# Kernel optimization log

Hardware: AMD Instinct MI355X
Metric: run time of the kernel (lower is better)

Reference implementation:

```python
import jax, jax.numpy as jnp
import numpy as np

EPS = float(jnp.finfo(jnp.float32).eps)


def _mlp(x, W1, b1, W2, b2, W3, b3):
    h = jax.nn.relu(x @ W1 + b1)
    h = jax.nn.relu(h @ W2 + b2)
    return h @ W3 + b3


def setup_inputs() -> dict:
    B, D_A, D_B, K, H = 131072, 16, 16, 32, 256
    key = jax.random.key(0)
    ks = jax.random.split(key, 13)
    def lin(k, fi, fo):
        return jax.random.normal(k, (fi, fo), jnp.float32) * (fi ** -0.5)
    inp = {
        "x": jax.random.uniform(ks[0], (B, D_A + D_B), jnp.float32),
        "hW1": lin(ks[1], D_A, H), "hb1": jnp.zeros((H,), jnp.float32),
        "hW2": lin(ks[2], H, H),   "hb2": jnp.zeros((H,), jnp.float32),
        "hW3": lin(ks[3], H, D_B * (K + 1)), "hb3": jnp.zeros((D_B * (K + 1),), jnp.float32),
        "wW1": lin(ks[4], D_A, H), "wb1": jnp.zeros((H,), jnp.float32),
        "wW2": lin(ks[5], H, H),   "wb2": jnp.zeros((H,), jnp.float32),
        "wW3": lin(ks[6], H, D_B * K), "wb3": jnp.zeros((D_B * K,), jnp.float32),
        "A_dims": jnp.arange(0, 32, 2, dtype=jnp.int32),
        "B_dims": jnp.arange(1, 32, 2, dtype=jnp.int32),
    }
    return inp


def reference(x, hW1, hb1, hW2, hb2, hW3, hb3, wW1, wb1, wW2, wb2, wW3, wb3, A_dims, B_dims):
    B = x.shape[0]
    D_B = B_dims.shape[0]
    K = wW3.shape[1] // D_B
    x_A = x[:, A_dims]               # (B, D_A)
    x_B = x[:, B_dims]               # (B, D_B)

    raw_h = _mlp(x_A, hW1, hb1, hW2, hb2, hW3, hb3).reshape(B, D_B, K + 1)
    heights = jax.nn.softplus(raw_h) + EPS
    raw_w = _mlp(x_A, wW1, wb1, wW2, wb2, wW3, wb3).reshape(B, D_B, K)
    widths = jax.nn.softmax(raw_w, axis=-1)
    zeros = jnp.zeros((B, D_B, 1), x.dtype)
    bins = jnp.concatenate([zeros, jnp.cumsum(widths, axis=-1)], axis=-1)  # (B, D_B, K+1)

    # preprocess_params_2: normalise PDF heights and bin areas
    bin_widths = bins[:, :, 1:] - bins[:, :, :-1]
    bin_areas = 0.5 * (heights[:, :, :-1] + heights[:, :, 1:]) * bin_widths  # (B, D_B, K)
    total_area = bin_areas.sum(axis=-1, keepdims=True)
    v = heights / total_area
    bin_areas = bin_areas / total_area

    # bin search
    i = jnp.sum(x_B[..., None] >= bins, axis=-1) - 1
    i = jnp.clip(i, 0, K - 1)                                  # (B, D_B)
    iu = i[..., None]

    x_left = jnp.take_along_axis(bins, iu, axis=2)[..., 0]
    x_right = jnp.take_along_axis(bins, iu + 1, axis=2)[..., 0]
    w_b = x_right - x_left
    v_left = jnp.take_along_axis(v, iu, axis=2)[..., 0]
    v_right = jnp.take_along_axis(v, iu + 1, axis=2)[..., 0]
    w_v = v_right - v_left

    alpha = (x_B - x_left) / (w_b + EPS)
    # cumulative area up to left edge of bin i: exclusive prefix sum then gather
    c_edges = jnp.concatenate([zeros, jnp.cumsum(bin_areas, axis=-1)], axis=-1)
    c_left = jnp.take_along_axis(c_edges, iu, axis=2)[..., 0]

    y_B = c_left + 0.5 * alpha ** 2 * w_v * w_b + alpha * v_left * w_b
    y = x.at[:, B_dims].set(y_B)
    return y
```

## Files before the change

kernel.cpp:

```cpp
#include <hip/hip_runtime.h>
#include <cmath>

typedef short short8 __attribute__((ext_vector_type(8)));
typedef short short4v __attribute__((ext_vector_type(4)));
typedef float f32x16 __attribute__((ext_vector_type(16)));

#define EPSF 1.1920929e-07f

#define LDS_A2W 0
#define LDS_A2H 33792
#define LDS_EW  67584
#define LDS_HH  104448
#define LDS_XA  67584
#define LDS_A1  69632
#define LDS_TOTAL 141312

#define OFF1H 0
#define OFF1W 4096
#define OFF2H 8192
#define OFF2W 73728
#define OFF3H 139264
#define OFF3W 278528

__device__ __forceinline__ unsigned short f2bf(float f) {
  union { float f; unsigned u; } v; v.f = f;
  return (unsigned short)((v.u + 0x8000u) >> 16);
}
__device__ __forceinline__ float bf2f(unsigned short h) {
  union { unsigned u; float f; } v; v.u = ((unsigned)h) << 16; return v.f;
}

__global__ void pack_weights(const float* __restrict__ hW1, const float* __restrict__ wW1,
                             const float* __restrict__ hW2, const float* __restrict__ wW2,
                             const float* __restrict__ hW3, const float* __restrict__ wW3,
                             unsigned short* __restrict__ out) {
  int tile = blockIdx.x, l = threadIdx.x;
  const float* src; unsigned short* dst; int NT, N, K, base;
  if (tile < 8)        { src = hW1; dst = out + OFF1H; NT = 8;  N = 256; K = 16;  base = tile; }
  else if (tile < 16)  { src = wW1; dst = out + OFF1W; NT = 8;  N = 256; K = 16;  base = tile - 8; }
  else if (tile < 144) { src = hW2; dst = out + OFF2H; NT = 8;  N = 256; K = 256; base = tile - 16; }
  else if (tile < 272) { src = wW2; dst = out + OFF2W; NT = 8;  N = 256; K = 256; base = tile - 144; }
  else if (tile < 544) { src = hW3; dst = out + OFF3H; NT = 17; N = 528; K = 256; base = tile - 272; }
  else                 { src = wW3; dst = out + OFF3W; NT = 16; N = 512; K = 256; base = tile - 544; }
  int nt = base % NT, kt = base / NT;
  int n = nt * 32 + (l & 31);
  int k0 = kt * 16 + (l >> 5) * 8;
  short8 v;
  #pragma unroll
  for (int e = 0; e < 8; e++) {
    float f = (n < N && (k0 + e) < K) ? src[(k0 + e) * N + n] : 0.f;
    v[e] = (short)f2bf(f);
  }
  *(short8*)(dst + (base * 64 + l) * 8) = v;
}

template <int KT, int NTB>
__device__ __forceinline__ f32x16 gemm_tile(const unsigned short* __restrict__ A, int apitch,
                                            const unsigned short* __restrict__ pB, int ct) {
  int l = threadIdx.x & 63;
  f32x16 acc = {0.f,0.f,0.f,0.f,0.f,0.f,0.f,0.f,0.f,0.f,0.f,0.f,0.f,0.f,0.f,0.f};
  const unsigned short* aptr = A + (l & 31) * apitch + (l >> 5) * 8;
  const unsigned short* bptr = pB + (ct * 64 + l) * 8;
  #pragma unroll
  for (int kt = 0; kt < KT; kt++) {
    short8 b = *(const short8*)(bptr + kt * (NTB * 512));
    short8 a = *(const short8*)(aptr + kt * 16);
    acc = __builtin_amdgcn_mfma_f32_32x32x16_bf16(a, b, acc, 0, 0, 0);
  }
  return acc;
}

__device__ __forceinline__ void epi_relu(char* lds, int oOff, f32x16 acc,
                                         const float* __restrict__ bias, int rt, int ct) {
  int l = threadIdx.x & 63;
  int col = ct * 32 + (l & 31);
  float bv = bias[col];
  unsigned short* o = (unsigned short*)(lds + oOff) + col + (rt * 32 + 4 * (l >> 5)) * 264;
  #pragma unroll
  for (int r = 0; r < 16; r++) {
    int row = (r & 3) + 8 * (r >> 2);
    o[row * 264] = f2bf(fmaxf(acc[r] + bv, 0.f));
  }
}

__global__ __launch_bounds__(1024, 4) void fused_kernel(
    const float* __restrict__ x,
    const float* __restrict__ hb1, const float* __restrict__ hb2, const float* __restrict__ hb3,
    const float* __restrict__ wb1, const float* __restrict__ wb2, const float* __restrict__ wb3,
    const unsigned short* __restrict__ pw,
    float* __restrict__ y) {
  extern __shared__ char lds[];
  const int t = threadIdx.x;
  const int w = t >> 6, l = t & 63;
  const int r0 = blockIdx.x * 64;

  if (t < 512) {
    int row = t >> 3, c4 = t & 7;
    float4 v = *(const float4*)(x + (r0 + row) * 32 + c4 * 4);
    y[(r0 + row) * 32 + c4 * 4] = v.x;
    y[(r0 + row) * 32 + c4 * 4 + 2] = v.z;
    unsigned short* xa = (unsigned short*)(lds + LDS_XA) + row * 16 + c4 * 2;
    xa[0] = f2bf(v.x); xa[1] = f2bf(v.z);
  }
  __syncthreads();

  const int rt = w >> 3, ct = w & 7;
  const unsigned short* XA = (const unsigned short*)(lds + LDS_XA);
  const unsigned short* A1 = (const unsigned short*)(lds + LDS_A1);
  const unsigned short* A2W = (const unsigned short*)(lds + LDS_A2W);
  const unsigned short* A2H = (const unsigned short*)(lds + LDS_A2H);

  { f32x16 a = gemm_tile<1, 8>(XA + rt * 32 * 16, 16, pw + OFF1W, ct);
    epi_relu(lds, LDS_A1, a, wb1, rt, ct); }
  __syncthreads();
  { f32x16 a = gemm_tile<16, 8>(A1 + rt * 32 * 264, 264, pw + OFF2W, ct);
    epi_relu(lds, LDS_A2W, a, wb2, rt, ct); }
  __syncthreads();
  { f32x16 a = gemm_tile<1, 8>(XA + rt * 32 * 16, 16, pw + OFF1H, ct);
    epi_relu(lds, LDS_A1, a, hb1, rt, ct); }
  __syncthreads();
  { f32x16 a = gemm_tile<16, 8>(A1 + rt * 32 * 264, 264, pw + OFF2H, ct);
    epi_relu(lds, LDS_A2H, a, hb2, rt, ct); }
  __syncthreads();

  #pragma unroll 1
  for (int H = 0; H < 2; H++) {
    for (int u = w; u < 34; u += 16) {
      int urt = u & 1, q = u >> 1;
      int rbase = urt * 32 + 4 * (l >> 5);
      if (q < 8) {
        int ctg = H * 8 + q;
        f32x16 a = gemm_tile<16, 16>(A2W + urt * 32 * 264, 264, pw + OFF3W, ctg);
        int c = ctg * 32 + (l & 31);
        float bv = wb3[c];
        unsigned short* o = (unsigned short*)(lds + LDS_EW) + rbase * 288 + (ctg & 7) * 36 + (l & 31);
        #pragma unroll
        for (int r = 0; r < 16; r++) {
          int row = (r & 3) + 8 * (r >> 2);
          o[row * 288] = f2bf(__expf(a[r] + bv));
        }
      } else {
        int ctg = (q - 8) + 8 * H;
        f32x16 a = gemm_tile<16, 17>(A2H + urt * 32 * 264, 264, pw + OFF3H, ctg);
        int c = ctg * 32 + (l & 31);
        if (c >= 264 * H && c < 264 * (H + 1)) {
          float bv = hb3[c];
          unsigned d = ((unsigned)c * 993u) >> 15;
          int j = c - 33 * (int)d;
          unsigned short* o = (unsigned short*)(lds + LDS_HH) + rbase * 288 + ((int)d & 7) * 36 + j;
          #pragma unroll
          for (int r = 0; r < 16; r++) {
            int row = (r & 3) + 8 * (r >> 2);
            float v = a[r] + bv;
            float sp = fmaxf(v, 0.f) + __logf(1.f + __expf(-fabsf(v))) + EPSF;
            o[row * 288] = f2bf(sp);
          }
        }
      }
    }
    __syncthreads();

    {
      int p = t >> 1, half = t & 1;
      int row = p >> 3, dl = p & 7, dg = H * 8 + dl;
      const unsigned short* EWp = (const unsigned short*)(lds + LDS_EW) + row * 288 + dl * 36 + half * 16;
      const unsigned short* HHp = (const unsigned short*)(lds + LDS_HH) + row * 288 + dl * 36 + half * 16;
      float e[16], hh[17];
      #pragma unroll
      for (int i = 0; i < 4; i++) {
        short4v ev = *(const short4v*)(EWp + i * 4);
        short4v hv = *(const short4v*)(HHp + i * 4);
        #pragma unroll
        for (int jj = 0; jj < 4; jj++) {
          e[i * 4 + jj] = bf2f((unsigned short)ev[jj]);
          hh[i * 4 + jj] = bf2f((unsigned short)hv[jj]);
        }
      }
      hh[16] = bf2f(HHp[16]);
      float se = 0.f;
      #pragma unroll
      for (int k = 0; k < 16; k++) se += e[k];
      float so = __shfl_xor(se, 1);
      float s = se + so;
      float bl = half ? so : 0.f;
      float xbv = x[(r0 + row) * 32 + 2 * dg + 1];
      float xbs = xbv * s;
      int fnd = (xbs >= bl) ? 1 : 0;
      float cl2 = 0.f, sxl = bl, sew = e[0], shl = hh[0], shr = hh[1], scl2 = 0.f;
      #pragma unroll
      for (int k = 0; k < 16; k++) {
        bool cond = (xbs >= bl);
        if (cond) { sxl = bl; sew = e[k]; shl = hh[k]; shr = hh[k + 1]; scl2 = cl2; }
        cl2 += (hh[k] + hh[k + 1]) * e[k];
        bl += e[k];
      }
      float cl2o = __shfl_xor(cl2, 1);
      float S2 = cl2 + cl2o;
      if (half) scl2 += cl2o;
      float o_sxl = __shfl_xor(sxl, 1), o_sew = __shfl_xor(sew, 1);
      float o_shl = __shfl_xor(shl, 1), o_shr = __shfl_xor(shr, 1);
      float o_scl2 = __shfl_xor(scl2, 1);
      int ofnd = __shfl_xor(fnd, 1);
      bool take_other = half ? (fnd == 0) : (ofnd != 0);
      if (take_other) { sxl = o_sxl; sew = o_sew; shl = o_shl; shr = o_shr; scl2 = o_scl2; }
      float alpha = (xbs - sxl) / (sew + EPSF);
      float yv = (scl2 + (alpha * alpha * (shr - shl) + 2.f * alpha * shl) * sew) / S2;
      if (!half) y[(r0 + row) * 32 + 2 * dg + 1] = yv;
    }
    __syncthreads();
  }
}

extern "C" void kernel_launch(void* const* d_in, const int* in_sizes, int n_in,
                              void* d_out, int out_size, void* d_ws, size_t ws_size,
                              hipStream_t stream) {
  const float* x   = (const float*)d_in[0];
  const float* hW1 = (const float*)d_in[1];
  const float* hb1 = (const float*)d_in[2];
  const float* hW2 = (const float*)d_in[3];
  const float* hb2 = (const float*)d_in[4];
  const float* hW3 = (const float*)d_in[5];
  const float* hb3 = (const float*)d_in[6];
  const float* wW1 = (const float*)d_in[7];
  const float* wb1 = (const float*)d_in[8];
  const float* wW2 = (const float*)d_in[9];
  const float* wb2 = (const float*)d_in[10];
  const float* wW3 = (const float*)d_in[11];
  const float* wb3 = (const float*)d_in[12];
  unsigned short* pw = (unsigned short*)d_ws;

  pack_weights<<<800, 64, 0, stream>>>(hW1, wW1, hW2, wW2, hW3, wW3, pw);

  hipFuncSetAttribute((const void*)fused_kernel,
                      hipFuncAttributeMaxDynamicSharedMemorySize, LDS_TOTAL);
  fused_kernel<<<2048, 1024, LDS_TOTAL, stream>>>(
      x, hb1, hb2, hb3, wb1, wb2, wb3, pw, (float*)d_out);
}
```

Before: 208.7 us.

## Halve block rows, shrink LDS, repack weights K-contiguous, fold bias into accumulator init

```diff
diff --git a/kernel.cpp b/kernel.cpp
--- a/kernel.cpp
+++ b/kernel.cpp
@@ -8,12 +8,13 @@
 #define EPSF 1.1920929e-07f
 
 #define LDS_A2W 0
-#define LDS_A2H 33792
-#define LDS_EW  67584
-#define LDS_HH  104448
-#define LDS_XA  67584
-#define LDS_A1  69632
-#define LDS_TOTAL 141312
+#define LDS_A2H 16896
+#define LDS_A1W 33792
+#define LDS_A1H 50688
+#define LDS_EW  33792
+#define LDS_HH  52224
+#define LDS_XA  70656
+#define LDS_TOTAL 71680
 
 #define OFF1H 0
 #define OFF1W 4096
@@ -42,7 +43,7 @@
   else if (tile < 272) { src = wW2; dst = out + OFF2W; NT = 8;  N = 256; K = 256; base = tile - 144; }
   else if (tile < 544) { src = hW3; dst = out + OFF3H; NT = 17; N = 528; K = 256; base = tile - 272; }
   else                 { src = wW3; dst = out + OFF3W; NT = 16; N = 512; K = 256; base = tile - 544; }
-  int nt = base % NT, kt = base / NT;
+  int nt = base % NT, kt = base / NT, KTT = K / 16;
   int n = nt * 32 + (l & 31);
   int k0 = kt * 16 + (l >> 5) * 8;
   short8 v;
@@ -51,39 +52,41 @@
     float f = (n < N && (k0 + e) < K) ? src[(k0 + e) * N + n] : 0.f;
     v[e] = (short)f2bf(f);
   }
-  *(short8*)(dst + (base * 64 + l) * 8) = v;
-}
-
-template <int KT, int NTB>
+  int idx = nt * KTT + kt;
+  *(short8*)(dst + (idx * 64 + l) * 8) = v;
+}
+
+template <int KT>
 __device__ __forceinline__ f32x16 gemm_tile(const unsigned short* __restrict__ A, int apitch,
-                                            const unsigned short* __restrict__ pB, int ct) {
+                                            const unsigned short* __restrict__ pB, int ct,
+                                            float init) {
   int l = threadIdx.x & 63;
-  f32x16 acc = {0.f,0.f,0.f,0.f,0.f,0.f,0.f,0.f,0.f,0.f,0.f,0.f,0.f,0.f,0.f,0.f};
+  f32x16 acc;
+  #pragma unroll
+  for (int r = 0; r < 16; r++) acc[r] = init;
   const unsigned short* aptr = A + (l & 31) * apitch + (l >> 5) * 8;
-  const unsigned short* bptr = pB + (ct * 64 + l) * 8;
+  const unsigned short* bptr = pB + (ct * KT * 64 + l) * 8;
   #pragma unroll
   for (int kt = 0; kt < KT; kt++) {
-    short8 b = *(const short8*)(bptr + kt * (NTB * 512));
+    short8 b = *(const short8*)(bptr + kt * 512);
     short8 a = *(const short8*)(aptr + kt * 16);
     acc = __builtin_amdgcn_mfma_f32_32x32x16_bf16(a, b, acc, 0, 0, 0);
   }
   return acc;
 }
 
-__device__ __forceinline__ void epi_relu(char* lds, int oOff, f32x16 acc,
-                                         const float* __restrict__ bias, int rt, int ct) {
+__device__ __forceinline__ void epi_relu(char* lds, int oOff, f32x16 acc, int ct) {
   int l = threadIdx.x & 63;
   int col = ct * 32 + (l & 31);
-  float bv = bias[col];
-  unsigned short* o = (unsigned short*)(lds + oOff) + col + (rt * 32 + 4 * (l >> 5)) * 264;
+  unsigned short* o = (unsigned short*)(lds + oOff) + col + 4 * (l >> 5) * 264;
   #pragma unroll
   for (int r = 0; r < 16; r++) {
     int row = (r & 3) + 8 * (r >> 2);
-    o[row * 264] = f2bf(fmaxf(acc[r] + bv, 0.f));
-  }
-}
-
-__global__ __launch_bounds__(1024, 4) void fused_kernel(
+    o[row * 264] = f2bf(fmaxf(acc[r], 0.f));
+  }
+}
+
+__global__ __launch_bounds__(512, 4) void fused_kernel(
     const float* __restrict__ x,
     const float* __restrict__ hb1, const float* __restrict__ hb2, const float* __restrict__ hb3,
     const float* __restrict__ wb1, const float* __restrict__ wb2, const float* __restrict__ wb3,
@@ -92,9 +95,9 @@
   extern __shared__ char lds[];
   const int t = threadIdx.x;
   const int w = t >> 6, l = t & 63;
-  const int r0 = blockIdx.x * 64;
-
-  if (t < 512) {
+  const int r0 = blockIdx.x * 32;
+
+  if (t < 256) {
     int row = t >> 3, c4 = t & 7;
     float4 v = *(const float4*)(x + (r0 + row) * 32 + c4 * 4);
     y[(r0 + row) * 32 + c4 * 4] = v.x;
@@ -104,54 +107,50 @@
   }
   __syncthreads();
 
-  const int rt = w >> 3, ct = w & 7;
-  const unsigned short* XA = (const unsigned short*)(lds + LDS_XA);
-  const unsigned short* A1 = (const unsigned short*)(lds + LDS_A1);
+  const unsigned short* XA  = (const unsigned short*)(lds + LDS_XA);
+  const unsigned short* A1W = (const unsigned short*)(lds + LDS_A1W);
+  const unsigned short* A1H = (const unsigned short*)(lds + LDS_A1H);
   const unsigned short* A2W = (const unsigned short*)(lds + LDS_A2W);
   const unsigned short* A2H = (const unsigned short*)(lds + LDS_A2H);
-
-  { f32x16 a = gemm_tile<1, 8>(XA + rt * 32 * 16, 16, pw + OFF1W, ct);
-    epi_relu(lds, LDS_A1, a, wb1, rt, ct); }
+  const int colw = w * 32 + (l & 31);
+
+  { f32x16 aw = gemm_tile<1>(XA, 16, pw + OFF1W, w, wb1[colw]);
+    epi_relu(lds, LDS_A1W, aw, w);
+    f32x16 ah = gemm_tile<1>(XA, 16, pw + OFF1H, w, hb1[colw]);
+    epi_relu(lds, LDS_A1H, ah, w); }
   __syncthreads();
-  { f32x16 a = gemm_tile<16, 8>(A1 + rt * 32 * 264, 264, pw + OFF2W, ct);
-    epi_relu(lds, LDS_A2W, a, wb2, rt, ct); }
-  __syncthreads();
-  { f32x16 a = gemm_tile<1, 8>(XA + rt * 32 * 16, 16, pw + OFF1H, ct);
-    epi_relu(lds, LDS_A1, a, hb1, rt, ct); }
-  __syncthreads();
-  { f32x16 a = gemm_tile<16, 8>(A1 + rt * 32 * 264, 264, pw + OFF2H, ct);
-    epi_relu(lds, LDS_A2H, a, hb2, rt, ct); }
+  { f32x16 aw = gemm_tile<16>(A1W, 264, pw + OFF2W, w, wb2[colw]);
+    epi_relu(lds, LDS_A2W, aw, w);
+    f32x16 ah = gemm_tile<16>(A1H, 264, pw + OFF2H, w, hb2[colw]);
+    epi_relu(lds, LDS_A2H, ah, w); }
   __syncthreads();
 
   #pragma unroll 1
   for (int H = 0; H < 2; H++) {
-    for (int u = w; u < 34; u += 16) {
-      int urt = u & 1, q = u >> 1;
-      int rbase = urt * 32 + 4 * (l >> 5);
-      if (q < 8) {
-        int ctg = H * 8 + q;
-        f32x16 a = gemm_tile<16, 16>(A2W + urt * 32 * 264, 264, pw + OFF3W, ctg);
-        int c = ctg * 32 + (l & 31);
-        float bv = wb3[c];
+    for (int u = w; u < 17; u += 8) {
+      int rbase = 4 * (l >> 5);
+      if (u < 8) {
+        int ctg = H * 8 + u;
+        f32x16 a = gemm_tile<16>(A2W, 264, pw + OFF3W, ctg, wb3[ctg * 32 + (l & 31)]);
         unsigned short* o = (unsigned short*)(lds + LDS_EW) + rbase * 288 + (ctg & 7) * 36 + (l & 31);
         #pragma unroll
         for (int r = 0; r < 16; r++) {
           int row = (r & 3) + 8 * (r >> 2);
-          o[row * 288] = f2bf(__expf(a[r] + bv));
+          o[row * 288] = f2bf(__expf(a[r]));
         }
       } else {
-        int ctg = (q - 8) + 8 * H;
-        f32x16 a = gemm_tile<16, 17>(A2H + urt * 32 * 264, 264, pw + OFF3H, ctg);
+        int ctg = (u - 8) + 8 * H;
         int c = ctg * 32 + (l & 31);
+        float bv = (c < 528) ? hb3[c] : 0.f;
+        f32x16 a = gemm_tile<16>(A2H, 264, pw + OFF3H, ctg, bv);
         if (c >= 264 * H && c < 264 * (H + 1)) {
-          float bv = hb3[c];
           unsigned d = ((unsigned)c * 993u) >> 15;
           int j = c - 33 * (int)d;
           unsigned short* o = (unsigned short*)(lds + LDS_HH) + rbase * 288 + ((int)d & 7) * 36 + j;
           #pragma unroll
           for (int r = 0; r < 16; r++) {
             int row = (r & 3) + 8 * (r >> 2);
-            float v = a[r] + bv;
+            float v = a[r];
             float sp = fmaxf(v, 0.f) + __logf(1.f + __expf(-fabsf(v))) + EPSF;
             o[row * 288] = f2bf(sp);
           }
@@ -163,8 +162,10 @@
     {
       int p = t >> 1, half = t & 1;
       int row = p >> 3, dl = p & 7, dg = H * 8 + dl;
-      const unsigned short* EWp = (const unsigned short*)(lds + LDS_EW) + row * 288 + dl * 36 + half * 16;
-      const unsigned short* HHp = (const unsigned short*)(lds + LDS_HH) + row * 288 + dl * 36 + half * 16;
+      const unsigned short* EWb = (const unsigned short*)(lds + LDS_EW) + row * 288 + dl * 36;
+      const unsigned short* HHb = (const unsigned short*)(lds + LDS_HH) + row * 288 + dl * 36;
+      const unsigned short* EWp = EWb + half * 16;
+      const unsigned short* HHp = HHb + half * 16;
       float e[16], hh[17];
       #pragma unroll
       for (int i = 0; i < 4; i++) {
@@ -182,29 +183,39 @@
       for (int k = 0; k < 16; k++) se += e[k];
       float so = __shfl_xor(se, 1);
       float s = se + so;
-      float bl = half ? so : 0.f;
       float xbv = x[(r0 + row) * 32 + 2 * dg + 1];
       float xbs = xbv * s;
-      int fnd = (xbs >= bl) ? 1 : 0;
-      float cl2 = 0.f, sxl = bl, sew = e[0], shl = hh[0], shr = hh[1], scl2 = 0.f;
+      float bl0 = half ? so : 0.f;
+      int fnd = (xbs >= bl0) ? 1 : 0;
+      float bl = bl0, cl2 = 0.f, sxl = bl0, scl2 = 0.f;
+      int ki = 0;
       #pragma unroll
       for (int k = 0; k < 16; k++) {
-        bool cond = (xbs >= bl);
-        if (cond) { sxl = bl; sew = e[k]; shl = hh[k]; shr = hh[k + 1]; scl2 = cl2; }
+        bool c = (xbs >= bl);
+        ki   = c ? k   : ki;
+        sxl  = c ? bl  : sxl;
+        scl2 = c ? cl2 : scl2;
         cl2 += (hh[k] + hh[k + 1]) * e[k];
-        bl += e[k];
+        bl  += e[k];
       }
       float cl2o = __shfl_xor(cl2, 1);
       float S2 = cl2 + cl2o;
       if (half) scl2 += cl2o;
-      float o_sxl = __shfl_xor(sxl, 1), o_sew = __shfl_xor(sew, 1);
-      float o_shl = __shfl_xor(shl, 1), o_shr = __shfl_xor(shr, 1);
+      int   o_ki   = __shfl_xor(ki, 1);
+      float o_sxl  = __shfl_xor(sxl, 1);
       float o_scl2 = __shfl_xor(scl2, 1);
-      int ofnd = __shfl_xor(fnd, 1);
-      bool take_other = half ? (fnd == 0) : (ofnd != 0);
-      if (take_other) { sxl = o_sxl; sew = o_sew; shl = o_shl; shr = o_shr; scl2 = o_scl2; }
-      float alpha = (xbs - sxl) / (sew + EPSF);
-      float yv = (scl2 + (alpha * alpha * (shr - shl) + 2.f * alpha * shl) * sew) / S2;
+      int   o_fnd  = __shfl_xor(fnd, 1);
+      bool other = half ? (fnd == 0) : (o_fnd != 0);
+      int   gki   = other ? o_ki   : ki;
+      int   ghalf = other ? (half ^ 1) : half;
+      float gsxl  = other ? o_sxl  : sxl;
+      float gscl2 = other ? o_scl2 : scl2;
+      int go = ghalf * 16 + gki;
+      float sew = bf2f(EWb[go]);
+      float shl = bf2f(HHb[go]);
+      float shr = bf2f(HHb[go + 1]);
+      float alpha = (xbs - gsxl) / (sew + EPSF);
+      float yv = (gscl2 + (alpha * alpha * (shr - shl) + 2.f * alpha * shl) * sew) / S2;
       if (!half) y[(r0 + row) * 32 + 2 * dg + 1] = yv;
     }
     __syncthreads();
@@ -233,6 +244,6 @@
 
   hipFuncSetAttribute((const void*)fused_kernel,
                       hipFuncAttributeMaxDynamicSharedMemorySize, LDS_TOTAL);
-  fused_kernel<<<2048, 1024, LDS_TOTAL, stream>>>(
+  fused_kernel<<<4096, 512, LDS_TOTAL, stream>>>(
       x, hb1, hb2, hb3, wb1, wb2, wb3, pw, (float*)d_out);
 }
```

After: 201.2 us. 3.6% less time.

## Transpose MFMA layout so spline params stay in registers, run both nets concurrently

Applied to the files above, without the earlier changes.

```diff
diff --git a/kernel.cpp b/kernel.cpp
--- a/kernel.cpp
+++ b/kernel.cpp
@@ -2,85 +2,80 @@
 #include <cmath>
 
 typedef short short8 __attribute__((ext_vector_type(8)));
-typedef short short4v __attribute__((ext_vector_type(4)));
 typedef float f32x16 __attribute__((ext_vector_type(16)));
 
 #define EPSF 1.1920929e-07f
 
-#define LDS_A2W 0
-#define LDS_A2H 33792
-#define LDS_EW  67584
-#define LDS_HH  104448
-#define LDS_XA  67584
-#define LDS_A1  69632
-#define LDS_TOTAL 141312
+#define LDS_XA  0
+#define LDS_A1H 3072
+#define LDS_A1W 36864
+#define LDS_A2H 70656
+#define LDS_A2W 104448
+#define LDS_H32 3072
+#define LDS_TOTAL 138240
 
 #define OFF1H 0
 #define OFF1W 4096
 #define OFF2H 8192
 #define OFF2W 73728
-#define OFF3H 139264
-#define OFF3W 278528
+#define OFF3W 139264
+#define OFF3H 270336
+#define OFFH32 401408
 
 __device__ __forceinline__ unsigned short f2bf(float f) {
   union { float f; unsigned u; } v; v.f = f;
   return (unsigned short)((v.u + 0x8000u) >> 16);
 }
-__device__ __forceinline__ float bf2f(unsigned short h) {
-  union { unsigned u; float f; } v; v.u = ((unsigned)h) << 16; return v.f;
+__device__ __forceinline__ float sp_eps(float v) {
+  return fmaxf(v, 0.f) + __logf(1.f + __expf(-fabsf(v))) + EPSF;
+}
+__device__ __forceinline__ int chanm(int m) {
+  return (((m >> 2) & 1) << 4) + (m & 3) + ((m >> 3) << 2);
 }
 
 __global__ void pack_weights(const float* __restrict__ hW1, const float* __restrict__ wW1,
                              const float* __restrict__ hW2, const float* __restrict__ wW2,
                              const float* __restrict__ hW3, const float* __restrict__ wW3,
                              unsigned short* __restrict__ out) {
-  int tile = blockIdx.x, l = threadIdx.x;
-  const float* src; unsigned short* dst; int NT, N, K, base;
-  if (tile < 8)        { src = hW1; dst = out + OFF1H; NT = 8;  N = 256; K = 16;  base = tile; }
-  else if (tile < 16)  { src = wW1; dst = out + OFF1W; NT = 8;  N = 256; K = 16;  base = tile - 8; }
-  else if (tile < 144) { src = hW2; dst = out + OFF2H; NT = 8;  N = 256; K = 256; base = tile - 16; }
-  else if (tile < 272) { src = wW2; dst = out + OFF2W; NT = 8;  N = 256; K = 256; base = tile - 144; }
-  else if (tile < 544) { src = hW3; dst = out + OFF3H; NT = 17; N = 528; K = 256; base = tile - 272; }
-  else                 { src = wW3; dst = out + OFF3W; NT = 16; N = 512; K = 256; base = tile - 544; }
-  int nt = base % NT, kt = base / NT;
-  int n = nt * 32 + (l & 31);
+  int bid = blockIdx.x, l = threadIdx.x;
+  int m = l & 31;
+  const float* W; unsigned short* dst; int tile, col, NC;
+  if (bid < 8)        { W = hW1; dst = out + OFF1H;  tile = bid;       col = tile * 32 + chanm(m); NC = 256; }
+  else if (bid < 16)  { W = wW1; dst = out + OFF1W;  tile = bid - 8;   col = tile * 32 + chanm(m); NC = 256; }
+  else if (bid < 144) { W = hW2; dst = out + OFF2H;  tile = bid - 16;  col = (tile >> 4) * 32 + chanm(m); NC = 256; }
+  else if (bid < 272) { W = wW2; dst = out + OFF2W;  tile = bid - 144; col = (tile >> 4) * 32 + chanm(m); NC = 256; }
+  else if (bid < 528) { W = wW3; dst = out + OFF3W;  tile = bid - 272; col = (tile >> 4) * 32 + chanm(m); NC = 512; }
+  else if (bid < 784) { W = hW3; dst = out + OFF3H;  tile = bid - 528; col = (tile >> 4) * 33 + chanm(m); NC = 528; }
+  else {
+    W = hW3; dst = out + OFFH32; tile = bid - 784;
+    int q = (m >> 2) & 1, rr = (m & 3) + ((m >> 3) << 2);
+    col = q ? -1 : rr * 33 + 32; NC = 528;
+  }
+  int kt = (bid < 16) ? 0 : (tile & 15);
+  int K  = (bid < 16) ? 16 : 256;
   int k0 = kt * 16 + (l >> 5) * 8;
   short8 v;
   #pragma unroll
   for (int e = 0; e < 8; e++) {
-    float f = (n < N && (k0 + e) < K) ? src[(k0 + e) * N + n] : 0.f;
+    float f = (col >= 0 && (k0 + e) < K) ? W[(k0 + e) * NC + col] : 0.f;
     v[e] = (short)f2bf(f);
   }
-  *(short8*)(dst + (base * 64 + l) * 8) = v;
-}
-
-template <int KT, int NTB>
-__device__ __forceinline__ f32x16 gemm_tile(const unsigned short* __restrict__ A, int apitch,
-                                            const unsigned short* __restrict__ pB, int ct) {
-  int l = threadIdx.x & 63;
-  f32x16 acc = {0.f,0.f,0.f,0.f,0.f,0.f,0.f,0.f,0.f,0.f,0.f,0.f,0.f,0.f,0.f,0.f};
-  const unsigned short* aptr = A + (l & 31) * apitch + (l >> 5) * 8;
-  const unsigned short* bptr = pB + (ct * 64 + l) * 8;
-  #pragma unroll
-  for (int kt = 0; kt < KT; kt++) {
-    short8 b = *(const short8*)(bptr + kt * (NTB * 512));
-    short8 a = *(const short8*)(aptr + kt * 16);
-    acc = __builtin_amdgcn_mfma_f32_32x32x16_bf16(a, b, acc, 0, 0, 0);
-  }
-  return acc;
-}
-
-__device__ __forceinline__ void epi_relu(char* lds, int oOff, f32x16 acc,
-                                         const float* __restrict__ bias, int rt, int ct) {
-  int l = threadIdx.x & 63;
-  int col = ct * 32 + (l & 31);
-  float bv = bias[col];
-  unsigned short* o = (unsigned short*)(lds + oOff) + col + (rt * 32 + 4 * (l >> 5)) * 264;
-  #pragma unroll
-  for (int r = 0; r < 16; r++) {
-    int row = (r & 3) + 8 * (r >> 2);
-    o[row * 264] = f2bf(fmaxf(acc[r] + bv, 0.f));
-  }
+  *(short8*)(dst + (tile * 64 + l) * 8) = v;
+}
+
+__device__ __forceinline__ void store_relu16(unsigned short* dstRow, f32x16 a) {
+  uint4 p0, p1;
+  unsigned pk[8];
+  #pragma unroll
+  for (int j = 0; j < 8; j++) {
+    unsigned lo = f2bf(fmaxf(a[2 * j], 0.f));
+    unsigned hi = f2bf(fmaxf(a[2 * j + 1], 0.f));
+    pk[j] = lo | (hi << 16);
+  }
+  p0.x = pk[0]; p0.y = pk[1]; p0.z = pk[2]; p0.w = pk[3];
+  p1.x = pk[4]; p1.y = pk[5]; p1.z = pk[6]; p1.w = pk[7];
+  *(uint4*)(dstRow) = p0;
+  *(uint4*)(dstRow + 8) = p1;
 }
 
 __global__ __launch_bounds__(1024, 4) void fused_kernel(
@@ -91,123 +86,170 @@
     float* __restrict__ y) {
   extern __shared__ char lds[];
   const int t = threadIdx.x;
-  const int w = t >> 6, l = t & 63;
+  const int w = t >> 6, l = t & 63, q = l >> 5, r32 = l & 31;
   const int r0 = blockIdx.x * 64;
+
+  unsigned short* XA  = (unsigned short*)(lds + LDS_XA);
+  unsigned short* A1H = (unsigned short*)(lds + LDS_A1H);
+  unsigned short* A1W = (unsigned short*)(lds + LDS_A1W);
+  unsigned short* A2H = (unsigned short*)(lds + LDS_A2H);
+  unsigned short* A2W = (unsigned short*)(lds + LDS_A2W);
+  float* H32 = (float*)(lds + LDS_H32);
 
   if (t < 512) {
     int row = t >> 3, c4 = t & 7;
     float4 v = *(const float4*)(x + (r0 + row) * 32 + c4 * 4);
     y[(r0 + row) * 32 + c4 * 4] = v.x;
     y[(r0 + row) * 32 + c4 * 4 + 2] = v.z;
-    unsigned short* xa = (unsigned short*)(lds + LDS_XA) + row * 16 + c4 * 2;
+    unsigned short* xa = XA + row * 24 + c4 * 2;
     xa[0] = f2bf(v.x); xa[1] = f2bf(v.z);
   }
   __syncthreads();
 
-  const int rt = w >> 3, ct = w & 7;
-  const unsigned short* XA = (const unsigned short*)(lds + LDS_XA);
-  const unsigned short* A1 = (const unsigned short*)(lds + LDS_A1);
-  const unsigned short* A2W = (const unsigned short*)(lds + LDS_A2W);
-  const unsigned short* A2H = (const unsigned short*)(lds + LDS_A2H);
-
-  { f32x16 a = gemm_tile<1, 8>(XA + rt * 32 * 16, 16, pw + OFF1W, ct);
-    epi_relu(lds, LDS_A1, a, wb1, rt, ct); }
-  __syncthreads();
-  { f32x16 a = gemm_tile<16, 8>(A1 + rt * 32 * 264, 264, pw + OFF2W, ct);
-    epi_relu(lds, LDS_A2W, a, wb2, rt, ct); }
-  __syncthreads();
-  { f32x16 a = gemm_tile<1, 8>(XA + rt * 32 * 16, 16, pw + OFF1H, ct);
-    epi_relu(lds, LDS_A1, a, hb1, rt, ct); }
-  __syncthreads();
-  { f32x16 a = gemm_tile<16, 8>(A1 + rt * 32 * 264, 264, pw + OFF2H, ct);
-    epi_relu(lds, LDS_A2H, a, hb2, rt, ct); }
-  __syncthreads();
-
-  #pragma unroll 1
-  for (int H = 0; H < 2; H++) {
-    for (int u = w; u < 34; u += 16) {
-      int urt = u & 1, q = u >> 1;
-      int rbase = urt * 32 + 4 * (l >> 5);
-      if (q < 8) {
-        int ctg = H * 8 + q;
-        f32x16 a = gemm_tile<16, 16>(A2W + urt * 32 * 264, 264, pw + OFF3W, ctg);
-        int c = ctg * 32 + (l & 31);
-        float bv = wb3[c];
-        unsigned short* o = (unsigned short*)(lds + LDS_EW) + rbase * 288 + (ctg & 7) * 36 + (l & 31);
-        #pragma unroll
-        for (int r = 0; r < 16; r++) {
-          int row = (r & 3) + 8 * (r >> 2);
-          o[row * 288] = f2bf(__expf(a[r] + bv));
-        }
-      } else {
-        int ctg = (q - 8) + 8 * H;
-        f32x16 a = gemm_tile<16, 17>(A2H + urt * 32 * 264, 264, pw + OFF3H, ctg);
-        int c = ctg * 32 + (l & 31);
-        if (c >= 264 * H && c < 264 * (H + 1)) {
-          float bv = hb3[c];
-          unsigned d = ((unsigned)c * 993u) >> 15;
-          int j = c - 33 * (int)d;
-          unsigned short* o = (unsigned short*)(lds + LDS_HH) + rbase * 288 + ((int)d & 7) * 36 + j;
-          #pragma unroll
-          for (int r = 0; r < 16; r++) {
-            int row = (r & 3) + 8 * (r >> 2);
-            float v = a[r] + bv;
-            float sp = fmaxf(v, 0.f) + __logf(1.f + __expf(-fabsf(v))) + EPSF;
-            o[row * 288] = f2bf(sp);
-          }
-        }
+  const int net = w >> 3, tc = w & 7;
+  unsigned short* A1n = net ? A1W : A1H;
+  unsigned short* A2n = net ? A2W : A2H;
+
+  {
+    const unsigned short* pA = pw + (net ? OFF1W : OFF1H) + tc * 512;
+    const float* b1 = net ? wb1 : hb1;
+    f32x16 a0, a1;
+    #pragma unroll
+    for (int rr = 0; rr < 16; rr++) { float bv = b1[tc * 32 + q * 16 + rr]; a0[rr] = bv; a1[rr] = bv; }
+    short8 af = *(const short8*)(pA + l * 8);
+    short8 b0 = *(const short8*)(XA + r32 * 24 + q * 8);
+    short8 b1f = *(const short8*)(XA + (32 + r32) * 24 + q * 8);
+    a0 = __builtin_amdgcn_mfma_f32_32x32x16_bf16(af, b0, a0, 0, 0, 0);
+    a1 = __builtin_amdgcn_mfma_f32_32x32x16_bf16(af, b1f, a1, 0, 0, 0);
+    store_relu16(A1n + r32 * 264 + tc * 32 + q * 16, a0);
+    store_relu16(A1n + (32 + r32) * 264 + tc * 32 + q * 16, a1);
+  }
+  __syncthreads();
+
+  {
+    const unsigned short* pA = pw + (net ? OFF2W : OFF2H) + tc * 16 * 512;
+    const float* b2 = net ? wb2 : hb2;
+    f32x16 a0, a1;
+    #pragma unroll
+    for (int rr = 0; rr < 16; rr++) { float bv = b2[tc * 32 + q * 16 + rr]; a0[rr] = bv; a1[rr] = bv; }
+    #pragma unroll
+    for (int kt = 0; kt < 16; kt++) {
+      short8 af = *(const short8*)(pA + kt * 512 + l * 8);
+      short8 b0 = *(const short8*)(A1n + r32 * 264 + kt * 16 + q * 8);
+      short8 b1f = *(const short8*)(A1n + (32 + r32) * 264 + kt * 16 + q * 8);
+      a0 = __builtin_amdgcn_mfma_f32_32x32x16_bf16(af, b0, a0, 0, 0, 0);
+      a1 = __builtin_amdgcn_mfma_f32_32x32x16_bf16(af, b1f, a1, 0, 0, 0);
+    }
+    store_relu16(A2n + r32 * 264 + tc * 32 + q * 16, a0);
+    store_relu16(A2n + (32 + r32) * 264 + tc * 32 + q * 16, a1);
+  }
+  __syncthreads();
+
+  const int d = w;
+  f32x16 ew0, ew1, hh0, hh1;
+  #pragma unroll
+  for (int rr = 0; rr < 16; rr++) {
+    float wv = wb3[d * 32 + q * 16 + rr];
+    float hv = hb3[d * 33 + q * 16 + rr];
+    ew0[rr] = wv; ew1[rr] = wv; hh0[rr] = hv; hh1[rr] = hv;
+  }
+  {
+    const unsigned short* pAW = pw + OFF3W + d * 16 * 512;
+    const unsigned short* pAH = pw + OFF3H + d * 16 * 512;
+    #pragma unroll
+    for (int kt = 0; kt < 16; kt++) {
+      short8 aw = *(const short8*)(pAW + kt * 512 + l * 8);
+      short8 bw0 = *(const short8*)(A2W + r32 * 264 + kt * 16 + q * 8);
+      short8 bw1 = *(const short8*)(A2W + (32 + r32) * 264 + kt * 16 + q * 8);
+      ew0 = __builtin_amdgcn_mfma_f32_32x32x16_bf16(aw, bw0, ew0, 0, 0, 0);
+      ew1 = __builtin_amdgcn_mfma_f32_32x32x16_bf16(aw, bw1, ew1, 0, 0, 0);
+      short8 ah = *(const short8*)(pAH + kt * 512 + l * 8);
+      short8 bh0 = *(const short8*)(A2H + r32 * 264 + kt * 16 + q * 8);
+      short8 bh1 = *(const short8*)(A2H + (32 + r32) * 264 + kt * 16 + q * 8);
+      hh0 = __builtin_amdgcn_mfma_f32_32x32x16_bf16(ah, bh0, hh0, 0, 0, 0);
+      hh1 = __builtin_amdgcn_mfma_f32_32x32x16_bf16(ah, bh1, hh1, 0, 0, 0);
+    }
+  }
+  #pragma unroll
+  for (int rr = 0; rr < 16; rr++) {
+    ew0[rr] = __expf(ew0[rr]); ew1[rr] = __expf(ew1[rr]);
+    hh0[rr] = sp_eps(hh0[rr]); hh1[rr] = sp_eps(hh1[rr]);
+  }
+  if (w >= 14) {
+    int rg = w - 14;
+    f32x16 a32;
+    #pragma unroll
+    for (int rr = 0; rr < 16; rr++) a32[rr] = 0.f;
+    const unsigned short* pA32 = pw + OFFH32;
+    #pragma unroll
+    for (int kt = 0; kt < 16; kt++) {
+      short8 af = *(const short8*)(pA32 + kt * 512 + l * 8);
+      short8 bf = *(const short8*)(A2H + (rg * 32 + r32) * 264 + kt * 16 + q * 8);
+      a32 = __builtin_amdgcn_mfma_f32_32x32x16_bf16(af, bf, a32, 0, 0, 0);
+    }
+    if (q == 0) {
+      float* o = H32 + (rg * 32 + r32) * 16;
+      #pragma unroll
+      for (int g = 0; g < 4; g++) {
+        float4 v;
+        v.x = sp_eps(a32[g * 4 + 0] + hb3[(g * 4 + 0) * 33 + 32]);
+        v.y = sp_eps(a32[g * 4 + 1] + hb3[(g * 4 + 1) * 33 + 32]);
+        v.z = sp_eps(a32[g * 4 + 2] + hb3[(g * 4 + 2) * 33 + 32]);
+        v.w = sp_eps(a32[g * 4 + 3] + hb3[(g * 4 + 3) * 33 + 32]);
+        *(float4*)(o + g * 4) = v;
       }
     }
-    __syncthreads();
-
-    {
-      int p = t >> 1, half = t & 1;
-      int row = p >> 3, dl = p & 7, dg = H * 8 + dl;
-      const unsigned short* EWp = (const unsigned short*)(lds + LDS_EW) + row * 288 + dl * 36 + half * 16;
-      const unsigned short* HHp = (const unsigned short*)(lds + LDS_HH) + row * 288 + dl * 36 + half * 16;
-      float e[16], hh[17];
-      #pragma unroll
-      for (int i = 0; i < 4; i++) {
-        short4v ev = *(const short4v*)(EWp + i * 4);
-        short4v hv = *(const short4v*)(HHp + i * 4);
-        #pragma unroll
-        for (int jj = 0; jj < 4; jj++) {
-          e[i * 4 + jj] = bf2f((unsigned short)ev[jj]);
-          hh[i * 4 + jj] = bf2f((unsigned short)hv[jj]);
-        }
-      }
-      hh[16] = bf2f(HHp[16]);
-      float se = 0.f;
-      #pragma unroll
-      for (int k = 0; k < 16; k++) se += e[k];
-      float so = __shfl_xor(se, 1);
-      float s = se + so;
-      float bl = half ? so : 0.f;
-      float xbv = x[(r0 + row) * 32 + 2 * dg + 1];
-      float xbs = xbv * s;
-      int fnd = (xbs >= bl) ? 1 : 0;
-      float cl2 = 0.f, sxl = bl, sew = e[0], shl = hh[0], shr = hh[1], scl2 = 0.f;
-      #pragma unroll
-      for (int k = 0; k < 16; k++) {
-        bool cond = (xbs >= bl);
-        if (cond) { sxl = bl; sew = e[k]; shl = hh[k]; shr = hh[k + 1]; scl2 = cl2; }
-        cl2 += (hh[k] + hh[k + 1]) * e[k];
-        bl += e[k];
-      }
-      float cl2o = __shfl_xor(cl2, 1);
-      float S2 = cl2 + cl2o;
-      if (half) scl2 += cl2o;
-      float o_sxl = __shfl_xor(sxl, 1), o_sew = __shfl_xor(sew, 1);
-      float o_shl = __shfl_xor(shl, 1), o_shr = __shfl_xor(shr, 1);
-      float o_scl2 = __shfl_xor(scl2, 1);
-      int ofnd = __shfl_xor(fnd, 1);
-      bool take_other = half ? (fnd == 0) : (ofnd != 0);
-      if (take_other) { sxl = o_sxl; sew = o_sew; shl = o_shl; shr = o_shr; scl2 = o_scl2; }
-      float alpha = (xbs - sxl) / (sew + EPSF);
-      float yv = (scl2 + (alpha * alpha * (shr - shl) + 2.f * alpha * shl) * sew) / S2;
-      if (!half) y[(r0 + row) * 32 + 2 * dg + 1] = yv;
-    }
-    __syncthreads();
+  }
+  __syncthreads();
+
+  #pragma unroll
+  for (int rg = 0; rg < 2; rg++) {
+    f32x16 e  = rg ? ew1 : ew0;
+    f32x16 hh = rg ? hh1 : hh0;
+    int row = rg * 32 + r32;
+    float se = 0.f;
+    #pragma unroll
+    for (int k = 0; k < 16; k++) se += e[k];
+    float so = __shfl_xor(se, 32);
+    float s = se + so;
+    float oth0 = __shfl_xor(hh[0], 32);
+    float h32v = H32[row * 16 + d];
+    float hh16 = q ? h32v : oth0;
+    float xbv = x[(r0 + row) * 32 + 2 * d + 1];
+    float xbs = xbv * s;
+    float bl = q ? so : 0.f;
+    int fnd = (xbs >= bl) ? 1 : 0;
+    float cl2 = 0.f, sxl = bl, sew = e[0], shl = hh[0], shr = hh[1], scl2 = 0.f;
+    #pragma unroll
+    for (int k = 0; k < 16; k++) {
+      float hn = (k < 15) ? hh[k + 1] : hh16;
+      bool c = (xbs >= bl);
+      sxl  = c ? bl    : sxl;
+      sew  = c ? e[k]  : sew;
+      shl  = c ? hh[k] : shl;
+      shr  = c ? hn    : shr;
+      scl2 = c ? cl2   : scl2;
+      cl2 += (hh[k] + hn) * e[k];
+      bl  += e[k];
+    }
+    float cl2o = __shfl_xor(cl2, 32);
+    float S2 = cl2 + cl2o;
+    if (q) scl2 += cl2o;
+    int   o_fnd  = __shfl_xor(fnd, 32);
+    float o_sxl  = __shfl_xor(sxl, 32);
+    float o_sew  = __shfl_xor(sew, 32);
+    float o_shl  = __shfl_xor(shl, 32);
+    float o_shr  = __shfl_xor(shr, 32);
+    float o_scl2 = __shfl_xor(scl2, 32);
+    bool other = q ? (fnd == 0) : (o_fnd != 0);
+    float gsxl  = other ? o_sxl  : sxl;
+    float gsew  = other ? o_sew  : sew;
+    float gshl  = other ? o_shl  : shl;
+    float gshr  = other ? o_shr  : shr;
+    float gscl2 = other ? o_scl2 : scl2;
+    float alpha = (xbs - gsxl) / (gsew + EPSF);
+    float yv = (gscl2 + (alpha * alpha * (gshr - gshl) + 2.f * alpha * gshl) * gsew) / S2;
+    if (q == 0) y[(r0 + row) * 32 + 2 * d + 1] = yv;
   }
 }
 
```

After: 199.5 us. 4.4% less time.
